# Kernel tuning notes

Measured on AMD Instinct MI355X. Metric: run time of the kernel, lower is better.

## Reference

```python
import jax, jax.numpy as jnp
import numpy as np

TOPK = 8  # n_activated_experts


def setup_inputs() -> dict:
    key = jax.random.key(0)
    k1, k2 = jax.random.split(key)
    tokens, dim, n_experts = 8192, 4096, 64
    x = jax.random.normal(k1, (tokens, dim), dtype=jnp.float32)
    weight = jax.random.normal(k2, (n_experts, dim), dtype=jnp.float32) * 0.02
    bias = jnp.zeros((n_experts,), dtype=jnp.float32)
    return {"x": x, "weight": weight, "bias": bias}


def reference(x, weight, bias):
    # scores: [tokens, n_experts]
    scores = jnp.einsum("td,ed->te", x, weight) + bias
    probs = jax.nn.softmax(scores, axis=-1)  # score_func == 'softmax'
    weights, indices = jax.lax.top_k(probs, TOPK)
    return probs, indices
```

## Files before the change

kernel.cpp:

```cpp
#include <hip/hip_runtime.h>
#include <math.h>

#define DIM     4096
#define NEXP    64
#define TOPK_N  8
#define TAU     2.0e-4f
#define TB      32
#define BK      128
#define KT      (DIM / BK)

#define WS_WHI_OFF  0
#define WS_WLO_OFF  524288

typedef __attribute__((ext_vector_type(8))) short short8;
typedef __attribute__((ext_vector_type(4))) float f32x4;

__device__ __forceinline__ void cvt8(float4 a0, float4 a1, short8& hv, short8& lv) {
    float f[8] = {a0.x, a0.y, a0.z, a0.w, a1.x, a1.y, a1.z, a1.w};
    union { short8 v; unsigned u[4]; } H, L;
    #pragma unroll
    for (int i = 0; i < 4; ++i) {
        unsigned b0 = __float_as_uint(f[2*i]);
        unsigned b1 = __float_as_uint(f[2*i+1]);
        float r0 = f[2*i]   - __uint_as_float(b0 & 0xffff0000u);
        float r1 = f[2*i+1] - __uint_as_float(b1 & 0xffff0000u);
        H.u[i] = (b0 >> 16) | (b1 & 0xffff0000u);
        L.u[i] = (__float_as_uint(r0) >> 16) | (__float_as_uint(r1) & 0xffff0000u);
    }
    hv = H.v; lv = L.v;
}

__device__ __forceinline__ void async16(void* lds, const void* g) {
    __builtin_amdgcn_global_load_lds(
        (const __attribute__((address_space(1))) unsigned int*)g,
        (__attribute__((address_space(3))) unsigned int*)lds, 16, 0, 0);
}

__global__ __launch_bounds__(256, 4)
void cvt_w_kernel(const float* __restrict__ w, unsigned short* __restrict__ whi,
                  unsigned short* __restrict__ wlo) {
    const int g = blockIdx.x * 256 + threadIdx.x;
    const float* p = w + (size_t)g * 8;
    union { short8 v; uint4 q; } H, L;
    float4 a0 = *(const float4*)(p);
    float4 a1 = *(const float4*)(p + 4);
    cvt8(a0, a1, H.v, L.v);
    *(uint4*)(whi + (size_t)g * 8) = H.q;
    *(uint4*)(wlo + (size_t)g * 8) = L.q;
}

__global__ __launch_bounds__(512, 2)
void gemm_kernel(const float* __restrict__ x, const unsigned short* __restrict__ whi,
                 const unsigned short* __restrict__ wlo, const float* __restrict__ bias,
                 const float* __restrict__ wfp, float* __restrict__ out, int ntok) {
    __shared__ struct {
        union {
            struct {
                float          A[2][TB][BK];
                unsigned short Bh[2][NEXP][BK];
                unsigned short Bl[2][NEXP][BK];
            } st;
            float part[4][TB][65];
        } u;
        float  s[TB][68];
        float  top9[TB][9];
        double dsc[NEXP];
        int    nflag;
        int    ftok[TB];
        float  fninth[TB];
    } sm;

    const int tid  = threadIdx.x;
    const int lane = tid & 63;
    const int wv   = tid >> 6;
    const int nl   = lane & 15;
    const int q    = lane >> 4;
    const int tok0 = blockIdx.x * TB;
    if (tid == 0) sm.nflag = 0;

    const int ss = wv & 3;
    const int hf = wv >> 2;
    const int abyte = ss * 128 + q * 32;
    const int bbyte = ss * 64 + q * 16;

    int arow0[2], be0[2];
    const float* gA[2];
    const unsigned short *gBh[2], *gBl[2];
    #pragma unroll
    for (int i = 0; i < 2; ++i) {
        arow0[i] = wv * 4 + i * 2;
        const int ra = arow0[i] + (lane >> 5);
        gA[i] = x + (size_t)(tok0 + ra) * DIM + (((lane & 31) * 4) ^ ((ra & 7) << 2));
        be0[i] = wv * 8 + i * 4;
        const int ea = be0[i] + (lane >> 4);
        const int el = (((lane & 15) * 8) ^ ((ea & 7) << 3));
        gBh[i] = whi + (size_t)ea * DIM + el;
        gBl[i] = wlo + (size_t)ea * DIM + el;
    }

    f32x4 acc[2][2];
    #pragma unroll
    for (int mg = 0; mg < 2; ++mg)
        #pragma unroll
        for (int nf = 0; nf < 2; ++nf) acc[mg][nf] = (f32x4){0.f, 0.f, 0.f, 0.f};

#define STAGE(b_, k0_) do {                                                    \
        _Pragma("unroll")                                                      \
        for (int i_ = 0; i_ < 2; ++i_) {                                       \
            async16(&sm.u.st.A[b_][arow0[i_]][0],  gA[i_]  + (k0_));           \
            async16(&sm.u.st.Bh[b_][be0[i_]][0],   gBh[i_] + (k0_));           \
            async16(&sm.u.st.Bl[b_][be0[i_]][0],   gBl[i_] + (k0_));           \
        }                                                                      \
    } while (0)

#define COMPUTE(b_) do {                                                       \
        short8 ahi_[2], alo_[2], bh_[2], bl_[2];                               \
        _Pragma("unroll")                                                      \
        for (int mg_ = 0; mg_ < 2; ++mg_) {                                    \
            const int r_ = mg_ * 16 + nl;                                      \
            const char* rp_ = (const char*)&sm.u.st.A[b_][r_][0];              \
            const int sw_ = (r_ & 7) << 4;                                     \
            float4 a0_ = *(const float4*)(rp_ + (abyte ^ sw_));                \
            float4 a1_ = *(const float4*)(rp_ + ((abyte + 16) ^ sw_));         \
            cvt8(a0_, a1_, ahi_[mg_], alo_[mg_]);                              \
        }                                                                      \
        _Pragma("unroll")                                                      \
        for (int nf_ = 0; nf_ < 2; ++nf_) {                                    \
            const int e_ = (hf * 2 + nf_) * 16 + nl;                           \
            const int sw_ = (e_ & 7) << 4;                                     \
            bh_[nf_] = *(const short8*)((const char*)&sm.u.st.Bh[b_][e_][0] + (bbyte ^ sw_)); \
            bl_[nf_] = *(const short8*)((const char*)&sm.u.st.Bl[b_][e_][0] + (bbyte ^ sw_)); \
        }                                                                      \
        _Pragma("unroll")                                                      \
        for (int mg_ = 0; mg_ < 2; ++mg_)                                      \
            _Pragma("unroll")                                                  \
            for (int nf_ = 0; nf_ < 2; ++nf_) {                                \
                acc[mg_][nf_] = __builtin_amdgcn_mfma_f32_16x16x32_bf16(ahi_[mg_], bl_[nf_], acc[mg_][nf_], 0, 0, 0); \
                acc[mg_][nf_] = __builtin_amdgcn_mfma_f32_16x16x32_bf16(alo_[mg_], bh_[nf_], acc[mg_][nf_], 0, 0, 0); \
                acc[mg_][nf_] = __builtin_amdgcn_mfma_f32_16x16x32_bf16(ahi_[mg_], bh_[nf_], acc[mg_][nf_], 0, 0, 0); \
            }                                                                  \
    } while (0)

    STAGE(0, 0);
    __syncthreads();
    #pragma unroll 2
    for (int kt = 0; kt < KT; ++kt) {
        const int b = kt & 1;
        if (kt + 1 < KT) STAGE(b ^ 1, (kt + 1) * BK);
        __builtin_amdgcn_sched_barrier(0);
        COMPUTE(b);
        __syncthreads();
    }

#undef STAGE
#undef COMPUTE

    #pragma unroll
    for (int mg = 0; mg < 2; ++mg)
        #pragma unroll
        for (int nf = 0; nf < 2; ++nf)
            #pragma unroll
            for (int r = 0; r < 4; ++r)
                sm.u.part[ss][mg * 16 + q * 4 + r][(hf * 2 + nf) * 16 + nl] = acc[mg][nf][r];
    __syncthreads();

    #pragma unroll
    for (int i = 0; i < (TB * NEXP) / 512; ++i) {
        const int p  = tid + i * 512;
        const int tk = p >> 6, e = p & 63;
        float s = sm.u.part[0][tk][e];
        #pragma unroll
        for (int k = 1; k < 4; ++k) s += sm.u.part[k][tk][e];
        sm.s[tk][e] = s + bias[e];
    }
    __syncthreads();

    float* __restrict__ out_idx = out + (size_t)ntok * NEXP;
    #pragma unroll
    for (int t = 0; t < 4; ++t) {
        const int tokl = wv * 4 + t;
        const int tok  = tok0 + tokl;
        const float s  = sm.s[tokl][lane];

        float m = s;
        #pragma unroll
        for (int off = 32; off > 0; off >>= 1)
            m = fmaxf(m, __shfl_xor(m, off, 64));
        const float ex = expf(s - m);
        float sum = ex;
        #pragma unroll
        for (int off = 32; off > 0; off >>= 1)
            sum += __shfl_xor(sum, off, 64);
        out[(size_t)tok * NEXP + lane] = ex / sum;

        int rank = 0;
        #pragma unroll
        for (int i = 0; i < 16; ++i) {
            const float4 v4 = *(const float4*)(&sm.s[tokl][i * 4]);
            rank += (int)((v4.x > s) || (v4.x == s && (i * 4 + 0) < lane));
            rank += (int)((v4.y > s) || (v4.y == s && (i * 4 + 1) < lane));
            rank += (int)((v4.z > s) || (v4.z == s && (i * 4 + 2) < lane));
            rank += (int)((v4.w > s) || (v4.w == s && (i * 4 + 3) < lane));
        }
        if (rank < TOPK_N + 1) sm.top9[tokl][rank] = s;
        if (rank < TOPK_N)
            out_idx[(size_t)tok * TOPK_N + rank] = (float)lane;
    }
    __syncthreads();

    if (tid < TB) {
        float ming = 1e30f;
        #pragma unroll
        for (int r = 0; r < TOPK_N; ++r)
            ming = fminf(ming, sm.top9[tid][r] - sm.top9[tid][r + 1]);
        if (ming < TAU) {
            const int sl = atomicAdd(&sm.nflag, 1);
            sm.ftok[sl] = tid;
            sm.fninth[sl] = sm.top9[tid][TOPK_N];
        }
    }
    __syncthreads();

    const int nfl = sm.nflag;
    for (int i = 0; i < nfl; ++i) {
        const int tokl = sm.ftok[i];
        const int tok  = tok0 + tokl;
        const float thr = sm.fninth[i] - TAU;
        const unsigned long long cmask = __ballot(sm.s[tokl][lane] >= thr);
        if (wv == 0) sm.dsc[lane] = -1.0e300;
        __syncthreads();
        {
            int rank = 0;
            unsigned long long mm = cmask;
            while (mm) {
                const int e = __builtin_ctzll(mm);
                mm &= mm - 1;
                if ((rank & 7) == wv) {
                    const float* wr  = wfp + (size_t)e * DIM;
                    const float* xrr = x + (size_t)tok * DIM;
                    double a = 0.0;
                    #pragma unroll 4
                    for (int kk = 0; kk < 16; ++kk) {
                        const int k = kk * 256 + lane * 4;
                        const float4 wv4 = *(const float4*)(wr + k);
                        const float4 xv  = *(const float4*)(xrr + k);
                        a = fma((double)xv.x, (double)wv4.x, a);
                        a = fma((double)xv.y, (double)wv4.y, a);
                        a = fma((double)xv.z, (double)wv4.z, a);
                        a = fma((double)xv.w, (double)wv4.w, a);
                    }
                    #pragma unroll
                    for (int off = 32; off > 0; off >>= 1)
                        a += __shfl_xor(a, off, 64);
                    if (lane == 0) sm.dsc[e] = a + (double)bias[e];
                }
                ++rank;
            }
        }
        __syncthreads();
        if (wv == 0) {
            double cv = sm.dsc[lane];
            for (int r = 0; r < TOPK_N; ++r) {
                double bv = cv;
                int    bi = lane;
                #pragma unroll
                for (int off = 32; off > 0; off >>= 1) {
                    const double ov = __shfl_xor(bv, off, 64);
                    const int    oi = __shfl_xor(bi, off, 64);
                    if (ov > bv || (ov == bv && oi < bi)) { bv = ov; bi = oi; }
                }
                if (lane == r)
                    out_idx[(size_t)tok * TOPK_N + r] = (float)bi;
                if (lane == bi) cv = -1.0e301;
            }
        }
        __syncthreads();
    }
}

extern "C" void kernel_launch(void* const* d_in, const int* in_sizes, int n_in,
                              void* d_out, int out_size, void* d_ws, size_t ws_size,
                              hipStream_t stream) {
    const float* x  = (const float*)d_in[0];
    const float* w  = (const float*)d_in[1];
    const float* bs = (const float*)d_in[2];
    float* out = (float*)d_out;

    unsigned short* whi = (unsigned short*)((char*)d_ws + WS_WHI_OFF);
    unsigned short* wlo = (unsigned short*)((char*)d_ws + WS_WLO_OFF);

    const int ntok = in_sizes[0] / DIM;

    hipLaunchKernelGGL(cvt_w_kernel, dim3((NEXP * DIM) / 8 / 256), dim3(256), 0, stream,
                       w, whi, wlo);
    hipLaunchKernelGGL(gemm_kernel, dim3(ntok / TB), dim3(512), 0, stream,
                       x, whi, wlo, bs, w, out, ntok);
}
```

Baseline: 251.9 us.

## Halve token tile, deepen K tile, and read expert weights straight from global

Each block now handles 16 tokens instead of 32 and uses a 512-wide K step, and only the activation tile is staged in shared memory. The bf16 hi/lo weight fragments are loaded directly from global memory (relying on L2/cache) rather than through LDS. This doubles the block count for better occupancy and cuts LDS traffic and staging. The cost is that weight reuse per block halves and the MFMA pipeline now waits on global-load latency for B.

```diff
diff --git a/kernel.cpp b/kernel.cpp
--- a/kernel.cpp
+++ b/kernel.cpp
@@ -5,9 +5,10 @@
 #define NEXP    64
 #define TOPK_N  8
 #define TAU     2.0e-4f
-#define TB      32
-#define BK      128
+#define TB      16
+#define BK      512
 #define KT      (DIM / BK)
+#define K32     4
 
 #define WS_WHI_OFF  0
 #define WS_WLO_OFF  524288
@@ -55,11 +56,7 @@
                  const float* __restrict__ wfp, float* __restrict__ out, int ntok) {
     __shared__ struct {
         union {
-            struct {
-                float          A[2][TB][BK];
-                unsigned short Bh[2][NEXP][BK];
-                unsigned short Bl[2][NEXP][BK];
-            } st;
+            float A[2][TB][BK];
             float part[4][TB][65];
         } u;
         float  s[TB][68];
@@ -80,65 +77,51 @@
 
     const int ss = wv & 3;
     const int hf = wv >> 2;
-    const int abyte = ss * 128 + q * 32;
-    const int bbyte = ss * 64 + q * 16;
-
-    int arow0[2], be0[2];
-    const float* gA[2];
-    const unsigned short *gBh[2], *gBl[2];
-    #pragma unroll
-    for (int i = 0; i < 2; ++i) {
-        arow0[i] = wv * 4 + i * 2;
-        const int ra = arow0[i] + (lane >> 5);
-        gA[i] = x + (size_t)(tok0 + ra) * DIM + (((lane & 31) * 4) ^ ((ra & 7) << 2));
-        be0[i] = wv * 8 + i * 4;
-        const int ea = be0[i] + (lane >> 4);
-        const int el = (((lane & 15) * 8) ^ ((ea & 7) << 3));
-        gBh[i] = whi + (size_t)ea * DIM + el;
-        gBl[i] = wlo + (size_t)ea * DIM + el;
-    }
-
-    f32x4 acc[2][2];
-    #pragma unroll
-    for (int mg = 0; mg < 2; ++mg)
-        #pragma unroll
-        for (int nf = 0; nf < 2; ++nf) acc[mg][nf] = (f32x4){0.f, 0.f, 0.f, 0.f};
-
-#define STAGE(b_, k0_) do {                                                    \
+
+    int arow[4], ahalf[4];
+    const float* gA[4];
+    #pragma unroll
+    for (int i = 0; i < 4; ++i) {
+        arow[i]  = wv * 2 + (i >> 1);
+        ahalf[i] = i & 1;
+        const int lb = ((lane * 16) ^ ((arow[i] & 7) << 4)) >> 2;
+        gA[i] = x + (size_t)(tok0 + arow[i]) * DIM + ahalf[i] * 256 + lb;
+    }
+
+    size_t boffB[2];
+    #pragma unroll
+    for (int nf = 0; nf < 2; ++nf) boffB[nf] = (size_t)((hf * 2 + nf) * 16 + nl) * DIM;
+
+    f32x4 acc[2];
+    acc[0] = (f32x4){0.f, 0.f, 0.f, 0.f};
+    acc[1] = (f32x4){0.f, 0.f, 0.f, 0.f};
+
+#define STAGE(b_, kf_) do {                                                    \
         _Pragma("unroll")                                                      \
-        for (int i_ = 0; i_ < 2; ++i_) {                                       \
-            async16(&sm.u.st.A[b_][arow0[i_]][0],  gA[i_]  + (k0_));           \
-            async16(&sm.u.st.Bh[b_][be0[i_]][0],   gBh[i_] + (k0_));           \
-            async16(&sm.u.st.Bl[b_][be0[i_]][0],   gBl[i_] + (k0_));           \
-        }                                                                      \
+        for (int i_ = 0; i_ < 4; ++i_)                                         \
+            async16(&sm.u.A[b_][arow[i_]][ahalf[i_] * 256], gA[i_] + (kf_));   \
     } while (0)
 
-#define COMPUTE(b_) do {                                                       \
-        short8 ahi_[2], alo_[2], bh_[2], bl_[2];                               \
+#define COMPUTE(b_, kf_) do {                                                  \
+        const char* rowp_ = (const char*)&sm.u.A[b_][nl][0];                   \
+        const int sw_ = (nl & 7) << 4;                                         \
         _Pragma("unroll")                                                      \
-        for (int mg_ = 0; mg_ < 2; ++mg_) {                                    \
-            const int r_ = mg_ * 16 + nl;                                      \
-            const char* rp_ = (const char*)&sm.u.st.A[b_][r_][0];              \
-            const int sw_ = (r_ & 7) << 4;                                     \
-            float4 a0_ = *(const float4*)(rp_ + (abyte ^ sw_));                \
-            float4 a1_ = *(const float4*)(rp_ + ((abyte + 16) ^ sw_));         \
-            cvt8(a0_, a1_, ahi_[mg_], alo_[mg_]);                              \
-        }                                                                      \
-        _Pragma("unroll")                                                      \
-        for (int nf_ = 0; nf_ < 2; ++nf_) {                                    \
-            const int e_ = (hf * 2 + nf_) * 16 + nl;                           \
-            const int sw_ = (e_ & 7) << 4;                                     \
-            bh_[nf_] = *(const short8*)((const char*)&sm.u.st.Bh[b_][e_][0] + (bbyte ^ sw_)); \
-            bl_[nf_] = *(const short8*)((const char*)&sm.u.st.Bl[b_][e_][0] + (bbyte ^ sw_)); \
-        }                                                                      \
-        _Pragma("unroll")                                                      \
-        for (int mg_ = 0; mg_ < 2; ++mg_)                                      \
+        for (int ks_ = 0; ks_ < K32; ++ks_) {                                  \
+            const int base_ = ss * 512 + ks_ * 128 + q * 32;                   \
+            float4 a0_ = *(const float4*)(rowp_ + (base_ ^ sw_));              \
+            float4 a1_ = *(const float4*)(rowp_ + ((base_ + 16) ^ sw_));       \
+            short8 ahi_, alo_;                                                 \
+            cvt8(a0_, a1_, ahi_, alo_);                                        \
+            const int kg_ = (kf_) + ss * 128 + ks_ * 32 + q * 8;               \
             _Pragma("unroll")                                                  \
             for (int nf_ = 0; nf_ < 2; ++nf_) {                                \
-                acc[mg_][nf_] = __builtin_amdgcn_mfma_f32_16x16x32_bf16(ahi_[mg_], bl_[nf_], acc[mg_][nf_], 0, 0, 0); \
-                acc[mg_][nf_] = __builtin_amdgcn_mfma_f32_16x16x32_bf16(alo_[mg_], bh_[nf_], acc[mg_][nf_], 0, 0, 0); \
-                acc[mg_][nf_] = __builtin_amdgcn_mfma_f32_16x16x32_bf16(ahi_[mg_], bh_[nf_], acc[mg_][nf_], 0, 0, 0); \
+                short8 bh_ = *(const short8*)(whi + boffB[nf_] + kg_);         \
+                short8 bl_ = *(const short8*)(wlo + boffB[nf_] + kg_);         \
+                acc[nf_] = __builtin_amdgcn_mfma_f32_16x16x32_bf16(ahi_, bl_, acc[nf_], 0, 0, 0); \
+                acc[nf_] = __builtin_amdgcn_mfma_f32_16x16x32_bf16(alo_, bh_, acc[nf_], 0, 0, 0); \
+                acc[nf_] = __builtin_amdgcn_mfma_f32_16x16x32_bf16(ahi_, bh_, acc[nf_], 0, 0, 0); \
             }                                                                  \
+        }                                                                      \
     } while (0)
 
     STAGE(0, 0);
@@ -148,7 +131,7 @@
         const int b = kt & 1;
         if (kt + 1 < KT) STAGE(b ^ 1, (kt + 1) * BK);
         __builtin_amdgcn_sched_barrier(0);
-        COMPUTE(b);
+        COMPUTE(b, kt * BK);
         __syncthreads();
     }
 
@@ -156,12 +139,10 @@
 #undef COMPUTE
 
     #pragma unroll
-    for (int mg = 0; mg < 2; ++mg)
-        #pragma unroll
-        for (int nf = 0; nf < 2; ++nf)
-            #pragma unroll
-            for (int r = 0; r < 4; ++r)
-                sm.u.part[ss][mg * 16 + q * 4 + r][(hf * 2 + nf) * 16 + nl] = acc[mg][nf][r];
+    for (int nf = 0; nf < 2; ++nf)
+        #pragma unroll
+        for (int r = 0; r < 4; ++r)
+            sm.u.part[ss][q * 4 + r][(hf * 2 + nf) * 16 + nl] = acc[nf][r];
     __syncthreads();
 
     #pragma unroll
@@ -177,8 +158,8 @@
 
     float* __restrict__ out_idx = out + (size_t)ntok * NEXP;
     #pragma unroll
-    for (int t = 0; t < 4; ++t) {
-        const int tokl = wv * 4 + t;
+    for (int t = 0; t < 2; ++t) {
+        const int tokl = wv * 2 + t;
         const int tok  = tok0 + tokl;
         const float s  = sm.s[tokl][lane];
 
```

Result: slower. 263.2 us (+4.5%).
